# Optimization experiments

Hardware: AMD Instinct MI355X
Metric: run time of the kernel (lower is better)

Reference implementation:

```python
import jax, jax.numpy as jnp
import numpy as np

B, TM1, E, D = 512, 256, 256, 256  # batch, T-1, encoder_hidden, decoder_hidden


def setup_inputs() -> dict:
    key = jax.random.key(0)
    ks = jax.random.split(key, 10)
    s = 0.05
    return {
        "input_encoded": jax.random.normal(ks[0], (B, TM1, E), dtype=jnp.float32),
        "y_history": jax.random.normal(ks[1], (B, TM1, 1), dtype=jnp.float32),
        # attn_layer: Linear(2D+E -> E), Tanh, Linear(E -> 1)
        "attn_w1": jax.random.normal(ks[2], (E, 2 * D + E), dtype=jnp.float32) * s,
        "attn_b1": jnp.zeros((E,), jnp.float32),
        "attn_w2": jax.random.normal(ks[3], (1, E), dtype=jnp.float32) * s,
        "attn_b2": jnp.zeros((1,), jnp.float32),
        # LSTM cell: input_size=1, hidden=D
        "W_ih": jax.random.normal(ks[4], (4 * D, 1), dtype=jnp.float32) * s,
        "W_hh": jax.random.normal(ks[5], (4 * D, D), dtype=jnp.float32) * s,
        "b_ih": jnp.zeros((4 * D,), jnp.float32),
        "b_hh": jnp.zeros((4 * D,), jnp.float32),
        # fc: Linear(E+1 -> 1), weight init normal_()
        "fc_w": jax.random.normal(ks[6], (1, E + 1), dtype=jnp.float32),
        "fc_b": jnp.zeros((1,), jnp.float32),
        # fc_final: Linear(D+E -> 2) (probabilistic)
        "fcf_w": jax.random.normal(ks[7], (2, D + E), dtype=jnp.float32) * s,
        "fcf_b": jnp.zeros((2,), jnp.float32),
    }


def _forward(input_encoded, y_history, attn_w1, attn_b1, attn_w2, attn_b2,
             W_ih, W_hh, b_ih, b_hh, fc_w, fc_b, fcf_w, fcf_b):
    # Split attn first linear into [hidden|cell] part and encoder part.
    w1_hc = attn_w1[:, : 2 * D]   # (E, 2D)
    w1_enc = attn_w1[:, 2 * D:]   # (E, E)
    # Encoder projection is invariant across timesteps: compute once. (B,TM1,E)
    enc_proj = jnp.einsum("bte,fe->btf", input_encoded, w1_enc) + attn_b1

    def step(carry, y_t):
        h, c, _ = carry  # h,c: (B,D); y_t: (B,1)
        hc = jnp.concatenate([h, c], axis=1)                     # (B, 2D)
        pre = jnp.tanh(enc_proj + (hc @ w1_hc.T)[:, None, :])    # (B, TM1, E)
        scores = jnp.einsum("bte,oe->bto", pre, attn_w2)[..., 0] + attn_b2[0]  # (B, TM1)
        alpha = jax.nn.softmax(scores, axis=1)
        context = jnp.einsum("bt,bte->be", alpha, input_encoded)  # (B, E)
        y_tilde = jnp.concatenate([context, y_t], axis=1) @ fc_w.T + fc_b  # (B,1)
        # LSTM cell (torch gate order: i, f, g, o)
        gates = y_tilde @ W_ih.T + b_ih + h @ W_hh.T + b_hh  # (B, 4D)
        i, f, g, o = jnp.split(gates, 4, axis=1)
        i = jax.nn.sigmoid(i); f = jax.nn.sigmoid(f)
        g = jnp.tanh(g); o = jax.nn.sigmoid(o)
        c_new = f * c + i * g
        h_new = o * jnp.tanh(c_new)
        return (h_new, c_new, context), None

    h0 = jnp.zeros((input_encoded.shape[0], D), input_encoded.dtype)
    c0 = jnp.zeros_like(h0)
    ctx0 = jnp.zeros((input_encoded.shape[0], E), input_encoded.dtype)
    ys = jnp.transpose(y_history, (1, 0, 2))  # (TM1, B, 1)
    (h, c, context), _ = jax.lax.scan(step, (h0, c0, ctx0), ys)
    return jnp.concatenate([h, context], axis=1) @ fcf_w.T + fcf_b  # (B, 2)


def reference(input_encoded, y_history, attn_w1, attn_b1, attn_w2, attn_b2,
              W_ih, W_hh, b_ih, b_hh, fc_w, fc_b, fcf_w, fcf_b):
    return _forward(input_encoded, y_history, attn_w1, attn_b1, attn_w2, attn_b2,
                    W_ih, W_hh, b_ih, b_hh, fc_w, fc_b, fcf_w, fcf_b)
```

## Files before the change

kernel.cpp:

```cpp
#include <hip/hip_runtime.h>
#include <cstdint>
#include <cstddef>


typedef _Float16 half8 __attribute__((ext_vector_type(8)));
typedef _Float16 half4v __attribute__((ext_vector_type(4)));
typedef _Float16 half2v __attribute__((ext_vector_type(2)));

__device__ __forceinline__ float rcpf_(float x) { return __builtin_amdgcn_rcpf(x); }
__device__ __forceinline__ float sigmoidf_(float x) { return rcpf_(1.f + __expf(-x)); }
__device__ __forceinline__ float tanhf_(float x) { return 1.f - 2.f * rcpf_(1.f + __expf(2.f * x)); }

#if defined(__has_builtin)
#if __has_builtin(__builtin_amdgcn_fdot2)
#define HAS_FDOT2 1
#endif
#endif
#ifndef HAS_FDOT2
#define HAS_FDOT2 0
#endif

__device__ __forceinline__ float fdot2_(half2v a, half2v b, float c) {
#if HAS_FDOT2
  return __builtin_amdgcn_fdot2(a, b, c, false);
#else
  return fmaf((float)a[0], (float)b[0], fmaf((float)a[1], (float)b[1], c));
#endif
}

__device__ __forceinline__ float dot8_(half8 w, half8 h, float acc) {
  acc = fdot2_(__builtin_shufflevector(w, w, 0, 1), __builtin_shufflevector(h, h, 0, 1), acc);
  acc = fdot2_(__builtin_shufflevector(w, w, 2, 3), __builtin_shufflevector(h, h, 2, 3), acc);
  acc = fdot2_(__builtin_shufflevector(w, w, 4, 5), __builtin_shufflevector(h, h, 4, 5), acc);
  acc = fdot2_(__builtin_shufflevector(w, w, 6, 7), __builtin_shufflevector(h, h, 6, 7), acc);
  return acc;
}


__global__ void k_prep_wT(const float* __restrict__ w1, float* __restrict__ wT) {
  int id = blockIdx.x * 256 + threadIdx.x;
  int e = id >> 8, f = id & 255;
  wT[id] = w1[f * 768 + 512 + e];
}

__global__ void k_prep_xh(const float* __restrict__ x, _Float16* __restrict__ xh) {
  int id = blockIdx.x * 256 + threadIdx.x;
  float4 v = reinterpret_cast<const float4*>(x)[id];
  half4v h;
  h[0] = (_Float16)v.x; h[1] = (_Float16)v.y; h[2] = (_Float16)v.z; h[3] = (_Float16)v.w;
  reinterpret_cast<half4v*>(xh)[id] = h;
}

__global__ void k_prep_w1hcQ(const float* __restrict__ w1, _Float16* __restrict__ o) {
  int id = blockIdx.x * 256 + threadIdx.x;
  int m = id & 7, t = (id >> 3) & 1023, c = id >> 13;
  int e = t & 255, jk = t >> 8;
  int k = jk * 128 + c * 8 + m;
  o[id] = (_Float16)w1[e * 768 + k];
}

__global__ void k_prep_whhG(const float* __restrict__ whh, _Float16* __restrict__ o) {
  int id = blockIdx.x * 256 + threadIdx.x;
  int m = id & 7, jo = (id >> 3) & 255, js = (id >> 11) & 3;
  int c = (id >> 13) & 15, kh = id >> 17;
  int j = js * 256 + jo, k = kh * 128 + c * 8 + m;
  o[id] = (_Float16)whh[j * 256 + k];
}

__global__ __launch_bounds__(256) void k_xf(const float* __restrict__ x,
                                            const float* __restrict__ fcw,
                                            float* __restrict__ xf) {
  __shared__ float xl[16][256];
  __shared__ float fw[256];
  __shared__ float part[16][17];
  const int tid = threadIdx.x;
  const int m0 = blockIdx.x * 16;
  fw[tid] = fcw[tid];
#pragma unroll
  for (int r = 0; r < 16; ++r) xl[r][tid] = x[(size_t)(m0 + r) * 256 + tid];
  __syncthreads();
  int r = tid >> 4, p = tid & 15;
  float s = 0.f;
#pragma unroll
  for (int u = 0; u < 16; ++u) s = fmaf(xl[r][p * 16 + u], fw[p * 16 + u], s);
  part[r][p] = s;
  __syncthreads();
  if (tid < 16) {
    float t = 0.f;
#pragma unroll
    for (int p2 = 0; p2 < 16; ++p2) t += part[tid][p2];
    xf[m0 + tid] = t;
  }
}

__global__ __launch_bounds__(256) void k_encp(const float* __restrict__ x,
                                              const float* __restrict__ wT,
                                              const float* __restrict__ b1,
                                              _Float16* __restrict__ Ph2) {
  __shared__ __align__(16) float xl[16][256];
  const int tid = threadIdx.x;
  const int m0 = blockIdx.x * 16;
#pragma unroll
  for (int r = 0; r < 16; ++r) xl[r][tid] = x[(size_t)(m0 + r) * 256 + tid];
  __syncthreads();
  float acc[16];
#pragma unroll
  for (int r = 0; r < 16; ++r) acc[r] = 0.f;
  for (int e = 0; e < 256; e += 4) {
    float w0 = wT[(e + 0) * 256 + tid];
    float w1_ = wT[(e + 1) * 256 + tid];
    float w2_ = wT[(e + 2) * 256 + tid];
    float w3_ = wT[(e + 3) * 256 + tid];
#pragma unroll
    for (int r = 0; r < 16; ++r) {
      float4 xv = *reinterpret_cast<const float4*>(&xl[r][e]);
      acc[r] = fmaf(xv.x, w0, acc[r]);
      acc[r] = fmaf(xv.y, w1_, acc[r]);
      acc[r] = fmaf(xv.z, w2_, acc[r]);
      acc[r] = fmaf(xv.w, w3_, acc[r]);
    }
  }
  float bb = b1[tid];
  const int e = tid;
#pragma unroll
  for (int r = 0; r < 16; ++r) {
    int m = m0 + r, b = m >> 8, t = m & 255;
    float p = __expf(2.f * (acc[r] + bb));
    Ph2[((size_t)(b * 32 + (e >> 3)) * 256 + t) * 8 + (e & 7)] = (_Float16)p;
  }
}

#define SC1(pv, c) { \
  float4 qa = q4[2*(c)], wa = w4[2*(c)]; \
  sacc0 = fmaf(wa.x, rcpf_(fmaf((float)pv[0], qa.x, 1.f)), sacc0); \
  sacc1 = fmaf(wa.y, rcpf_(fmaf((float)pv[1], qa.y, 1.f)), sacc1); \
  sacc0 = fmaf(wa.z, rcpf_(fmaf((float)pv[2], qa.z, 1.f)), sacc0); \
  sacc1 = fmaf(wa.w, rcpf_(fmaf((float)pv[3], qa.w, 1.f)), sacc1); \
  float4 qb = q4[2*(c)+1], wb = w4[2*(c)+1]; \
  sacc0 = fmaf(wb.x, rcpf_(fmaf((float)pv[4], qb.x, 1.f)), sacc0); \
  sacc1 = fmaf(wb.y, rcpf_(fmaf((float)pv[5], qb.y, 1.f)), sacc1); \
  sacc0 = fmaf(wb.z, rcpf_(fmaf((float)pv[6], qb.z, 1.f)), sacc0); \
  sacc1 = fmaf(wb.w, rcpf_(fmaf((float)pv[7], qb.w, 1.f)), sacc1); }

__global__ __launch_bounds__(1024, 4) void k_scan(
    const _Float16* __restrict__ Ph2, const _Float16* __restrict__ xh,
    const _Float16* __restrict__ w1hcQ, const _Float16* __restrict__ whhG,
    const float* __restrict__ xf, const float* __restrict__ y_hist,
    const float* __restrict__ w2g, const float* __restrict__ Wih,
    const float* __restrict__ bih, const float* __restrict__ bhh,
    const float* __restrict__ fcw, const float* __restrict__ fcb,
    const float* __restrict__ fcfw, const float* __restrict__ fcfb,
    float* __restrict__ out) {
  __shared__ __align__(16) float hc[2][512];
  __shared__ __align__(16) _Float16 hcH[2][512];
  __shared__ __align__(16) float qpart[4][2][256];
  __shared__ __align__(16) float Qs[2][256];
  __shared__ __align__(16) float spart[2][2][256];
  __shared__ __align__(16) float ealpha[2][256];
  __shared__ __align__(16) float gpart[2][2][1024];
  __shared__ __align__(16) _Float16 PhL[2][12][256][8];
  __shared__ __align__(16) float w2l[256];
  __shared__ __align__(16) float Wihl[1024];
  __shared__ __align__(16) float bl[1024];
  __shared__ __align__(16) float xfL[2][256];
  __shared__ __align__(16) float yhL[2][256];
  __shared__ float redA[8], redB[8];

  const int tid = threadIdx.x;
  const int b0 = blockIdx.x * 2;
  const int hi = tid >> 8;
  const int lo = tid & 255;
  const int wv = tid >> 6, lane = tid & 63;

  ((float*)hc)[tid] = 0.f;
  ((_Float16*)hcH)[tid] = (_Float16)0.f;
  if (tid < 256) w2l[tid] = w2g[tid];
  Wihl[tid & 1023] = Wih[tid & 1023];
  bl[tid] = bih[tid] + bhh[tid];
  if (tid < 512) {
    int gi = tid >> 8, ti = tid & 255;
    xfL[gi][ti] = xf[(size_t)(b0 + gi) * 256 + ti];
    yhL[gi][ti] = y_hist[(size_t)(b0 + gi) * 256 + ti];
  }
  {
    half8* phl8 = reinterpret_cast<half8*>(&PhL[0][0][0][0]);
    const half8* ph8 = reinterpret_cast<const half8*>(Ph2);
#pragma unroll
    for (int u = 0; u < 6; ++u) {
      int slot = u * 1024 + tid;
      int g = slot >= 3072;
      int rem = slot - g * 3072;
      int ci = rem >> 8;
      int t = rem & 255;
      int cc = (ci < 6) ? (2 * ci) : (16 + 2 * (ci - 6));
      phl8[slot] = ph8[((size_t)(b0 + g) * 32 + cc) * 256 + t];
    }
  }
  __syncthreads();
  float w2sum = 0.f;
  for (int e2 = 0; e2 < 256; ++e2) w2sum += w2l[e2];
  const float fcb0 = fcb[0];
  const float fcwy = fcw[256];

  const half8* wq = reinterpret_cast<const half8*>(w1hcQ) + tid;
  const int kh = hi & 1, jp = hi >> 1;
  const half8* wg = reinterpret_cast<const half8*>(whhG) + (size_t)kh * 16384 + jp * 512 + lo;
  const int gs = tid >> 9, eh = (tid >> 8) & 1;
  const half8* prow = reinterpret_cast<const half8*>(Ph2) +
                      ((size_t)((b0 + gs) * 32 + eh * 16)) * 256 + lo;
  const half8* phlR = reinterpret_cast<const half8*>(&PhL[0][0][0][0]) +
                      (gs * 12 + eh * 6) * 256 + lo;
  const int gp = (tid >> 8) & 1;

#pragma unroll 1
  for (int s = 0; s < 256; ++s) {
    float a0 = 0.f, a1 = 0.f;
    {
      const half8* hp0 = reinterpret_cast<const half8*>(&hcH[0][hi * 128]);
      const half8* hp1 = reinterpret_cast<const half8*>(&hcH[1][hi * 128]);
#pragma unroll 8
      for (int c = 0; c < 16; ++c) {
        half8 w = wq[c * 1024];
        half8 h0 = hp0[c];
        half8 h1 = hp1[c];
        a0 = dot8_(w, h0, a0);
        a1 = dot8_(w, h1, a1);
      }
    }
    qpart[hi][0][lo] = a0;
    qpart[hi][1][lo] = a1;
    __syncthreads();

    if (tid < 512) {
      float qv = qpart[0][gp][lo] + qpart[1][gp][lo] + qpart[2][gp][lo] + qpart[3][gp][lo];
      Qs[gp][lo] = __expf(2.f * qv);
    }
    float ac00 = 0.f, ac01 = 0.f, ac10 = 0.f, ac11 = 0.f;
    {
      const half8* hg0 = reinterpret_cast<const half8*>(&hcH[0][kh * 128]);
      const half8* hg1 = reinterpret_cast<const half8*>(&hcH[1][kh * 128]);
#pragma unroll 4
      for (int c = 0; c < 16; ++c) {
        half8 h0 = hg0[c];
        half8 h1 = hg1[c];
        half8 w0 = wg[c * 1024];
        half8 w1v = wg[c * 1024 + 256];
        ac00 = dot8_(w0, h0, ac00);  ac10 = dot8_(w0, h1, ac10);
        ac01 = dot8_(w1v, h0, ac01); ac11 = dot8_(w1v, h1, ac11);
      }
    }
    gpart[kh][0][(jp * 2 + 0) * 256 + lo] = ac00;
    gpart[kh][0][(jp * 2 + 1) * 256 + lo] = ac01;
    gpart[kh][1][(jp * 2 + 0) * 256 + lo] = ac10;
    gpart[kh][1][(jp * 2 + 1) * 256 + lo] = ac11;
    __syncthreads();

    float sacc0 = 0.f, sacc1 = 0.f;
    {
      const float4* q4 = reinterpret_cast<const float4*>(&Qs[gs][eh * 128]);
      const float4* w4 = reinterpret_cast<const float4*>(&w2l[eh * 128]);
      half8 s1 = prow[1 * 256];
      half8 s3 = prow[3 * 256];
      half8 s5 = prow[5 * 256];
      half8 s7 = prow[7 * 256];
      half8 s9 = prow[9 * 256];
      half8 s11 = prow[11 * 256];
      half8 s12 = prow[12 * 256];
      half8 s13 = prow[13 * 256];
      half8 s14 = prow[14 * 256];
      half8 s15 = prow[15 * 256];
      { half8 l0 = phlR[0 * 256];  SC1(l0, 0) }
      { half8 l2 = phlR[1 * 256];  SC1(l2, 2) }
      { half8 l4 = phlR[2 * 256];  SC1(l4, 4) }
      { half8 l6 = phlR[3 * 256];  SC1(l6, 6) }
      { half8 l8 = phlR[4 * 256];  SC1(l8, 8) }
      { half8 la = phlR[5 * 256];  SC1(la, 10) }
      SC1(s1, 1)  SC1(s3, 3)  SC1(s5, 5)  SC1(s7, 7)  SC1(s9, 9)
      SC1(s11, 11) SC1(s12, 12) SC1(s13, 13) SC1(s14, 14) SC1(s15, 15)
    }
    spart[eh][gs][lo] = sacc0 + sacc1;
    __syncthreads();

    if (tid < 512) {
      float sc = w2sum - 2.f * (spart[0][gp][lo] + spart[1][gp][lo]);
      float ea = __expf(sc);
      ealpha[gp][lo] = ea;
      float ef = ea * xfL[gp][lo];
      float es = ea;
#pragma unroll
      for (int off = 32; off > 0; off >>= 1) {
        es += __shfl_xor(es, off);
        ef += __shfl_xor(ef, off);
      }
      if (lane == 0) { redA[wv] = es; redB[wv] = ef; }
    }
    __syncthreads();

    if (tid < 512) {
      float es = (gp == 0) ? (redA[0] + redA[1] + redA[2] + redA[3])
                           : (redA[4] + redA[5] + redA[6] + redA[7]);
      float ef = (gp == 0) ? (redB[0] + redB[1] + redB[2] + redB[3])
                           : (redB[4] + redB[5] + redB[6] + redB[7]);
      float yt = ef * rcpf_(es) + fmaf(yhL[gp][s], fcwy, fcb0);
      float gi = fmaf(yt, Wihl[lo], bl[lo]);
      float gf = fmaf(yt, Wihl[256 + lo], bl[256 + lo]);
      float gc = fmaf(yt, Wihl[512 + lo], bl[512 + lo]);
      float go = fmaf(yt, Wihl[768 + lo], bl[768 + lo]);
      gi += gpart[0][gp][lo] + gpart[1][gp][lo];
      gf += gpart[0][gp][256 + lo] + gpart[1][gp][256 + lo];
      gc += gpart[0][gp][512 + lo] + gpart[1][gp][512 + lo];
      go += gpart[0][gp][768 + lo] + gpart[1][gp][768 + lo];
      float iv = sigmoidf_(gi), fv = sigmoidf_(gf), gv = tanhf_(gc), ov = sigmoidf_(go);
      float cold = hc[gp][256 + lo];
      float cn = fmaf(fv, cold, iv * gv);
      float hn = ov * tanhf_(cn);
      hc[gp][lo] = hn;
      hc[gp][256 + lo] = cn;
      hcH[gp][lo] = (_Float16)hn;
      hcH[gp][256 + lo] = (_Float16)cn;
    }
    __syncthreads();
  }

  const float rsA = rcpf_(redA[0] + redA[1] + redA[2] + redA[3]);
  const float rsB = rcpf_(redA[4] + redA[5] + redA[6] + redA[7]);

  float* cpartF = reinterpret_cast<float*>(&PhL[0][0][0][0]);
  {
    const int gc = tid >> 9, t16 = (tid >> 5) & 15, l5 = tid & 31;
    const half8* xrow = reinterpret_cast<const half8*>(xh) +
                        ((size_t)(b0 + gc) * 256 + t16 * 16) * 32 + l5;
    float acx[8];
#pragma unroll
    for (int m = 0; m < 8; ++m) acx[m] = 0.f;
#pragma unroll 4
    for (int it = 0; it < 16; ++it) {
      float al = ealpha[gc][t16 * 16 + it];
      half8 xv = xrow[it * 32];
#pragma unroll
      for (int m = 0; m < 8; ++m) acx[m] = fmaf(al, (float)xv[m], acx[m]);
    }
    float* dst = &cpartF[((gc * 16 + t16) * 256) + l5 * 8];
    *reinterpret_cast<float4*>(dst) = *reinterpret_cast<float4*>(&acx[0]);
    *reinterpret_cast<float4*>(dst + 4) = *reinterpret_cast<float4*>(&acx[4]);
  }
  __syncthreads();

  if (tid < 512) {
    float cv = 0.f;
#pragma unroll
    for (int u = 0; u < 16; ++u) cv += cpartF[((gp * 16 + u) * 256) + lo];
    cv *= (gp == 0) ? rsA : rsB;
    float hval = hc[gp][lo];
    float p0 = hval * fcfw[lo] + cv * fcfw[256 + lo];
    float p1 = hval * fcfw[512 + lo] + cv * fcfw[768 + lo];
#pragma unroll
    for (int off = 32; off > 0; off >>= 1) {
      p0 += __shfl_xor(p0, off);
      p1 += __shfl_xor(p1, off);
    }
    if (lane == 0) { redA[wv] = p0; redB[wv] = p1; }
  }
  __syncthreads();
  if (tid < 4) {
    int g2 = tid >> 1, o = tid & 1;
    const float* r = (o == 0) ? redA : redB;
    float v = fcfb[o] + r[g2 * 4 + 0] + r[g2 * 4 + 1] + r[g2 * 4 + 2] + r[g2 * 4 + 3];
    out[(b0 + g2) * 2 + o] = v;
  }
}

extern "C" void kernel_launch(void* const* d_in, const int* in_sizes, int n_in,
                              void* d_out, int out_size, void* d_ws, size_t ws_size,
                              hipStream_t stream) {
  (void)in_sizes; (void)n_in; (void)out_size; (void)ws_size;
  const float* x    = (const float*)d_in[0];
  const float* yh   = (const float*)d_in[1];
  const float* w1   = (const float*)d_in[2];
  const float* b1   = (const float*)d_in[3];
  const float* w2   = (const float*)d_in[4];
  const float* Wih  = (const float*)d_in[6];
  const float* Whh  = (const float*)d_in[7];
  const float* bih  = (const float*)d_in[8];
  const float* bhh  = (const float*)d_in[9];
  const float* fcw  = (const float*)d_in[10];
  const float* fcb  = (const float*)d_in[11];
  const float* fcfw = (const float*)d_in[12];
  const float* fcfb = (const float*)d_in[13];
  float* out = (float*)d_out;

  char* ws = (char*)d_ws;
  _Float16* Ph2   = (_Float16*)(ws);
  _Float16* xh    = (_Float16*)(ws + (size_t)67108864);
  float*    wT    = (float*)   (ws + (size_t)134217728);
  _Float16* w1hcQ = (_Float16*)(ws + (size_t)134479872);
  _Float16* whhG  = (_Float16*)(ws + (size_t)134742016);
  float*    xf    = (float*)   (ws + (size_t)135266304);

  k_prep_wT   <<<256,   256, 0, stream>>>(w1, wT);
  k_prep_xh   <<<32768, 256, 0, stream>>>(x, xh);
  k_prep_w1hcQ<<<512,   256, 0, stream>>>(w1, w1hcQ);
  k_prep_whhG <<<1024,  256, 0, stream>>>(Whh, whhG);
  k_xf        <<<8192,  256, 0, stream>>>(x, fcw, xf);
  k_encp      <<<8192,  256, 0, stream>>>(x, wT, b1, Ph2);
  k_scan      <<<256,  1024, 0, stream>>>(Ph2, xh, w1hcQ, whhG, xf, yh, w2, Wih,
                                          bih, bhh, fcw, fcb, fcfw, fcfb, out);
}
```

Baseline: 4.078 ms.

## Split Q and gate matvecs across thread halves to remove a barrier

The hidden-state projections for attention (Q) and the LSTM gates now run in parallel on separate thread halves. Threads 0-511 compute Q with a two-lane shuffle reduction, and threads 512-1023 compute the full-K gate dot products. This removes the qpart and gpart partial buffers and one __syncthreads per step, and the weight pre-layout kernels change to match. The shared memory freed is used to cache one more Ph2 chunk in LDS, leaving one fewer global load in the score loop. The cost is that each thread half now does twice the serial work, which lengthens the critical path per step and may leave the two halves unevenly loaded.

```diff
diff --git a/kernel.cpp b/kernel.cpp
--- a/kernel.cpp
+++ b/kernel.cpp
@@ -53,18 +53,15 @@
 
 __global__ void k_prep_w1hcQ(const float* __restrict__ w1, _Float16* __restrict__ o) {
   int id = blockIdx.x * 256 + threadIdx.x;
-  int m = id & 7, t = (id >> 3) & 1023, c = id >> 13;
-  int e = t & 255, jk = t >> 8;
-  int k = jk * 128 + c * 8 + m;
-  o[id] = (_Float16)w1[e * 768 + k];
+  int m = id & 7, lane = (id >> 3) & 511, c = id >> 12;
+  int e = lane >> 1, kh = lane & 1;
+  o[id] = (_Float16)w1[e * 768 + kh * 256 + c * 8 + m];
 }
 
 __global__ void k_prep_whhG(const float* __restrict__ whh, _Float16* __restrict__ o) {
   int id = blockIdx.x * 256 + threadIdx.x;
-  int m = id & 7, jo = (id >> 3) & 255, js = (id >> 11) & 3;
-  int c = (id >> 13) & 15, kh = id >> 17;
-  int j = js * 256 + jo, k = kh * 128 + c * 8 + m;
-  o[id] = (_Float16)whh[j * 256 + k];
+  int m = id & 7, j = (id >> 3) & 1023, c = id >> 13;
+  o[id] = (_Float16)whh[j * 256 + c * 8 + m];
 }
 
 __global__ __launch_bounds__(256) void k_xf(const float* __restrict__ x,
@@ -153,12 +150,11 @@
     float* __restrict__ out) {
   __shared__ __align__(16) float hc[2][512];
   __shared__ __align__(16) _Float16 hcH[2][512];
-  __shared__ __align__(16) float qpart[4][2][256];
   __shared__ __align__(16) float Qs[2][256];
   __shared__ __align__(16) float spart[2][2][256];
   __shared__ __align__(16) float ealpha[2][256];
-  __shared__ __align__(16) float gpart[2][2][1024];
-  __shared__ __align__(16) _Float16 PhL[2][12][256][8];
+  __shared__ __align__(16) float gfull[2][1024];
+  __shared__ __align__(16) _Float16 PhL[2][14][256][8];
   __shared__ __align__(16) float w2l[256];
   __shared__ __align__(16) float Wihl[1024];
   __shared__ __align__(16) float bl[1024];
@@ -168,7 +164,6 @@
 
   const int tid = threadIdx.x;
   const int b0 = blockIdx.x * 2;
-  const int hi = tid >> 8;
   const int lo = tid & 255;
   const int wv = tid >> 6, lane = tid & 63;
 
@@ -186,13 +181,13 @@
     half8* phl8 = reinterpret_cast<half8*>(&PhL[0][0][0][0]);
     const half8* ph8 = reinterpret_cast<const half8*>(Ph2);
 #pragma unroll
-    for (int u = 0; u < 6; ++u) {
-      int slot = u * 1024 + tid;
-      int g = slot >= 3072;
-      int rem = slot - g * 3072;
+    for (int u2 = 0; u2 < 7; ++u2) {
+      int slot = u2 * 1024 + tid;
+      int g = slot >= 3584;
+      int rem = slot - g * 3584;
       int ci = rem >> 8;
       int t = rem & 255;
-      int cc = (ci < 6) ? (2 * ci) : (16 + 2 * (ci - 6));
+      int cc = (ci < 7) ? (2 * ci) : (16 + 2 * (ci - 7));
       phl8[slot] = ph8[((size_t)(b0 + g) * 32 + cc) * 256 + t];
     }
   }
@@ -202,57 +197,54 @@
   const float fcb0 = fcb[0];
   const float fcwy = fcw[256];
 
-  const half8* wq = reinterpret_cast<const half8*>(w1hcQ) + tid;
-  const int kh = hi & 1, jp = hi >> 1;
-  const half8* wg = reinterpret_cast<const half8*>(whhG) + (size_t)kh * 16384 + jp * 512 + lo;
+  const half8* wq2 = reinterpret_cast<const half8*>(w1hcQ) + tid;
+  const int khq = tid & 1;
+  const int ug = (tid - 512) & 511;
+  const half8* wgJ = reinterpret_cast<const half8*>(whhG) + ug;
   const int gs = tid >> 9, eh = (tid >> 8) & 1;
   const half8* prow = reinterpret_cast<const half8*>(Ph2) +
                       ((size_t)((b0 + gs) * 32 + eh * 16)) * 256 + lo;
   const half8* phlR = reinterpret_cast<const half8*>(&PhL[0][0][0][0]) +
-                      (gs * 12 + eh * 6) * 256 + lo;
+                      (gs * 14 + eh * 7) * 256 + lo;
   const int gp = (tid >> 8) & 1;
 
 #pragma unroll 1
   for (int s = 0; s < 256; ++s) {
-    float a0 = 0.f, a1 = 0.f;
-    {
-      const half8* hp0 = reinterpret_cast<const half8*>(&hcH[0][hi * 128]);
-      const half8* hp1 = reinterpret_cast<const half8*>(&hcH[1][hi * 128]);
+    if (tid < 512) {
+      float a0 = 0.f, a1 = 0.f;
+      const half8* hp0 = reinterpret_cast<const half8*>(&hcH[0][khq * 256]);
+      const half8* hp1 = reinterpret_cast<const half8*>(&hcH[1][khq * 256]);
 #pragma unroll 8
-      for (int c = 0; c < 16; ++c) {
-        half8 w = wq[c * 1024];
-        half8 h0 = hp0[c];
-        half8 h1 = hp1[c];
-        a0 = dot8_(w, h0, a0);
-        a1 = dot8_(w, h1, a1);
+      for (int c = 0; c < 32; ++c) {
+        half8 w = wq2[c * 512];
+        a0 = dot8_(w, hp0[c], a0);
+        a1 = dot8_(w, hp1[c], a1);
       }
-    }
-    qpart[hi][0][lo] = a0;
-    qpart[hi][1][lo] = a1;
-    __syncthreads();
-
-    if (tid < 512) {
-      float qv = qpart[0][gp][lo] + qpart[1][gp][lo] + qpart[2][gp][lo] + qpart[3][gp][lo];
-      Qs[gp][lo] = __expf(2.f * qv);
-    }
-    float ac00 = 0.f, ac01 = 0.f, ac10 = 0.f, ac11 = 0.f;
-    {
-      const half8* hg0 = reinterpret_cast<const half8*>(&hcH[0][kh * 128]);
-      const half8* hg1 = reinterpret_cast<const half8*>(&hcH[1][kh * 128]);
+      a0 += __shfl_xor(a0, 1);
+      a1 += __shfl_xor(a1, 1);
+      if (khq == 0) {
+        int e = tid >> 1;
+        Qs[0][e] = __expf(2.f * a0);
+        Qs[1][e] = __expf(2.f * a1);
+      }
+    } else {
+      float ac00 = 0.f, ac01 = 0.f, ac10 = 0.f, ac11 = 0.f;
+      const half8* hg0 = reinterpret_cast<const half8*>(&hcH[0][0]);
+      const half8* hg1 = reinterpret_cast<const half8*>(&hcH[1][0]);
 #pragma unroll 4
-      for (int c = 0; c < 16; ++c) {
+      for (int c = 0; c < 32; ++c) {
         half8 h0 = hg0[c];
         half8 h1 = hg1[c];
-        half8 w0 = wg[c * 1024];
-        half8 w1v = wg[c * 1024 + 256];
-        ac00 = dot8_(w0, h0, ac00);  ac10 = dot8_(w0, h1, ac10);
-        ac01 = dot8_(w1v, h0, ac01); ac11 = dot8_(w1v, h1, ac11);
+        half8 w0 = wgJ[c * 1024];
+        half8 w1v = wgJ[c * 1024 + 512];
+        ac00 = dot8_(w0, h0, ac00);  ac01 = dot8_(w0, h1, ac01);
+        ac10 = dot8_(w1v, h0, ac10); ac11 = dot8_(w1v, h1, ac11);
       }
-    }
-    gpart[kh][0][(jp * 2 + 0) * 256 + lo] = ac00;
-    gpart[kh][0][(jp * 2 + 1) * 256 + lo] = ac01;
-    gpart[kh][1][(jp * 2 + 0) * 256 + lo] = ac10;
-    gpart[kh][1][(jp * 2 + 1) * 256 + lo] = ac11;
+      gfull[0][ug] = ac00;
+      gfull[1][ug] = ac01;
+      gfull[0][ug + 512] = ac10;
+      gfull[1][ug + 512] = ac11;
+    }
     __syncthreads();
 
     float sacc0 = 0.f, sacc1 = 0.f;
@@ -265,7 +257,6 @@
       half8 s7 = prow[7 * 256];
       half8 s9 = prow[9 * 256];
       half8 s11 = prow[11 * 256];
-      half8 s12 = prow[12 * 256];
       half8 s13 = prow[13 * 256];
       half8 s14 = prow[14 * 256];
       half8 s15 = prow[15 * 256];
@@ -275,8 +266,9 @@
       { half8 l6 = phlR[3 * 256];  SC1(l6, 6) }
       { half8 l8 = phlR[4 * 256];  SC1(l8, 8) }
       { half8 la = phlR[5 * 256];  SC1(la, 10) }
+      { half8 lc = phlR[6 * 256];  SC1(lc, 12) }
       SC1(s1, 1)  SC1(s3, 3)  SC1(s5, 5)  SC1(s7, 7)  SC1(s9, 9)
-      SC1(s11, 11) SC1(s12, 12) SC1(s13, 13) SC1(s14, 14) SC1(s15, 15)
+      SC1(s11, 11) SC1(s13, 13) SC1(s14, 14) SC1(s15, 15)
     }
     spart[eh][gs][lo] = sacc0 + sacc1;
     __syncthreads();
@@ -302,14 +294,10 @@
       float ef = (gp == 0) ? (redB[0] + redB[1] + redB[2] + redB[3])
                            : (redB[4] + redB[5] + redB[6] + redB[7]);
       float yt = ef * rcpf_(es) + fmaf(yhL[gp][s], fcwy, fcb0);
-      float gi = fmaf(yt, Wihl[lo], bl[lo]);
-      float gf = fmaf(yt, Wihl[256 + lo], bl[256 + lo]);
-      float gc = fmaf(yt, Wihl[512 + lo], bl[512 + lo]);
-      float go = fmaf(yt, Wihl[768 + lo], bl[768 + lo]);
-      gi += gpart[0][gp][lo] + gpart[1][gp][lo];
-      gf += gpart[0][gp][256 + lo] + gpart[1][gp][256 + lo];
-      gc += gpart[0][gp][512 + lo] + gpart[1][gp][512 + lo];
-      go += gpart[0][gp][768 + lo] + gpart[1][gp][768 + lo];
+      float gi = fmaf(yt, Wihl[lo], bl[lo]) + gfull[gp][lo];
+      float gf = fmaf(yt, Wihl[256 + lo], bl[256 + lo]) + gfull[gp][256 + lo];
+      float gc = fmaf(yt, Wihl[512 + lo], bl[512 + lo]) + gfull[gp][512 + lo];
+      float go = fmaf(yt, Wihl[768 + lo], bl[768 + lo]) + gfull[gp][768 + lo];
       float iv = sigmoidf_(gi), fv = sigmoidf_(gf), gv = tanhf_(gc), ov = sigmoidf_(go);
       float cold = hc[gp][256 + lo];
       float cn = fmaf(fv, cold, iv * gv);
```

Result: faster. 3.722 ms (-8.7%).
